# Performance work log

Hardware: AMD Instinct MI355X
Metric: run time of the kernel (lower is better)

The kernel has to match this reference:

```python
import jax, jax.numpy as jnp
import numpy as np

B, NPTS, T, P, C, D = 2, 32768, 32768, 512, 4, 768


def _sincos_pos_embed(centers, embed_dim):
    # centers: np [P,3]; matches get_3d_sincos_pos_embed
    c = centers - centers.mean(axis=0)
    c = c / np.linalg.norm(c, axis=1).max()
    div = np.exp(np.arange(0, embed_dim, 6) * -(np.log(10000.0) / embed_dim))  # [D/6]
    arg = c[:, None, :] * div[None, :, None]                                   # [P, D/6, 3]
    pe = np.concatenate([np.sin(arg), np.cos(arg)], axis=-1).reshape(centers.shape[0], embed_dim)
    return pe.astype(np.float32)


def setup_inputs() -> dict:
    key = jax.random.key(0)
    ks = jax.random.split(key, 12)
    rng = np.random.default_rng(0)

    # ragged patch sizes (avg 64) summing exactly to T
    sizes = rng.integers(32, 97, size=P).astype(np.int64)
    sizes = np.maximum((sizes * (T / sizes.sum())).astype(np.int64), 1)
    sizes[-1] += T - sizes.sum()
    patch_offset = jnp.asarray(np.concatenate([[0], np.cumsum(sizes)]), dtype=jnp.int32)  # [P+1]

    patch_index = jax.random.randint(ks[0], (T,), 0, NPTS, dtype=jnp.int32)
    latent = jax.random.normal(ks[1], (B, NPTS, C), dtype=jnp.float32)

    s = 0.02
    params = dict(
        w1a=jax.random.normal(ks[2], (C, D), jnp.float32) * s,
        b1a=jnp.zeros((D,), jnp.float32),
        w1b=jax.random.normal(ks[3], (D, D), jnp.float32) * s,
        b1b=jnp.zeros((D,), jnp.float32),
        w2a=jax.random.normal(ks[4], (2 * D, D), jnp.float32) * s,
        b2a=jnp.zeros((D,), jnp.float32),
        g2=jnp.ones((D,), jnp.float32),
        beta2=jnp.zeros((D,), jnp.float32),
        w2b=jax.random.normal(ks[5], (D, D), jnp.float32) * s,
        b2b=jnp.zeros((D,), jnp.float32),
    )

    centers = rng.standard_normal((P, 3))
    pos_embed = jnp.asarray(_sincos_pos_embed(centers, D))[None]  # [1, P, D]

    return dict(latent=latent, patch_index=patch_index, patch_offset=patch_offset,
                pos_embed=pos_embed, **params)


def _ln(x, eps, gamma=None, beta=None):
    mu = x.mean(axis=-1, keepdims=True)
    var = ((x - mu) ** 2).mean(axis=-1, keepdims=True)
    y = (x - mu) * jax.lax.rsqrt(var + eps)
    if gamma is not None:
        y = y * gamma + beta
    return y


def reference(latent, patch_index, patch_offset, pos_embed,
              w1a, b1a, w1b, b1b, w2a, b2a, g2, beta2, w2b, b2b):
    T_ = patch_index.shape[0]
    P_ = patch_offset.shape[0] - 1
    # segment id of each token (repeat_interleave inverse): seg[t] = patch containing t
    seg = jnp.searchsorted(patch_offset[1:], jnp.arange(T_, dtype=patch_offset.dtype), side='right')

    x = latent[:, patch_index, :]                           # [B, T, C] gather
    h = x @ w1a + b1a
    h = jax.nn.gelu(_ln(h, 1e-6), approximate=False)
    h = h @ w1b + b1b                                       # [B, T, D]

    segmax = lambda a: jax.ops.segment_max(a, seg, num_segments=P_)
    y = jax.vmap(segmax)(h)                                 # [B, P, D] ragged max-pool

    h2 = jnp.concatenate([y[:, seg, :], h], axis=-1)        # repeat_interleave + concat
    h2 = h2 @ w2a + b2a
    h2 = jax.nn.gelu(_ln(h2, 1e-5, g2, beta2), approximate=False)
    h2 = h2 @ w2b + b2b                                     # [B, T, D]
    raw_latent = h2

    out = jax.vmap(segmax)(raw_latent) + pos_embed          # [B, P, D]
    return out.astype(raw_latent.dtype), raw_latent
```

## Files before the change

kernel.cpp:

```cpp
#include <hip/hip_runtime.h>
#include <hip/hip_bf16.h>
#include <math.h>

#define B_    2
#define NPTS_ 32768
#define T_    32768
#define P_    512
#define C_    4
#define D_    768
#define M_    (B_ * T_)

typedef __bf16 bf16_t;
typedef __bf16 bf16x8 __attribute__((ext_vector_type(8)));
typedef __bf16 bf16x4 __attribute__((ext_vector_type(4)));
typedef float  f32x4  __attribute__((ext_vector_type(4)));

__device__ inline void gload16(const void* g, void* l) {
  __builtin_amdgcn_global_load_lds(
      (const __attribute__((address_space(1))) void*)g,
      (__attribute__((address_space(3))) void*)l, 16, 0, 0);
}

__device__ inline float gelu_exact(float x) {
  return 0.5f * x * (1.0f + erff(x * 0.70710678118654752f));
}

__device__ inline unsigned fmap(float x) {
  unsigned u = __float_as_uint(x);
  return (u & 0x80000000u) ? ~u : (u | 0x80000000u);
}
__device__ inline float funmap(unsigned u) {
  unsigned v = (u & 0x80000000u) ? (u & 0x7FFFFFFFu) : ~u;
  return __uint_as_float(v);
}

__global__ __launch_bounds__(256) void bigprep_kernel(
    const float4* __restrict__ latent4, const int* __restrict__ pidx,
    const float* __restrict__ w1a, const float* __restrict__ b1a,
    bf16_t* __restrict__ act1,
    const int* __restrict__ off, int* __restrict__ seg, uint4* __restrict__ umax,
    const float* __restrict__ w1b, const float* __restrict__ w2a,
    const float* __restrict__ w2b, const float* __restrict__ b1b,
    bf16_t* __restrict__ wBig, bf16_t* __restrict__ w2aTT,
    bf16_t* __restrict__ w2aBT, bf16_t* __restrict__ w2bT,
    bf16_t* __restrict__ w1bR, float* __restrict__ bBig) {
  int bid = blockIdx.x, tid = threadIdx.x;
  if (bid < 4096) {
    int wid = tid >> 6, lane = tid & 63;
    int mb = bid * 16 + wid * 4;
    int d8 = lane * 8, d4 = 512 + lane * 4;
    float bb[12], wreg[4][12];
    {
      float4 a0 = *(const float4*)(b1a + d8);
      float4 a1 = *(const float4*)(b1a + d8 + 4);
      float4 a2 = *(const float4*)(b1a + d4);
      bb[0]=a0.x; bb[1]=a0.y; bb[2]=a0.z; bb[3]=a0.w;
      bb[4]=a1.x; bb[5]=a1.y; bb[6]=a1.z; bb[7]=a1.w;
      bb[8]=a2.x; bb[9]=a2.y; bb[10]=a2.z; bb[11]=a2.w;
    }
    #pragma unroll
    for (int k = 0; k < 4; ++k) {
      const float* w = w1a + k * D_;
      float4 w0 = *(const float4*)(w + d8);
      float4 w1 = *(const float4*)(w + d8 + 4);
      float4 w2 = *(const float4*)(w + d4);
      wreg[k][0]=w0.x; wreg[k][1]=w0.y; wreg[k][2]=w0.z; wreg[k][3]=w0.w;
      wreg[k][4]=w1.x; wreg[k][5]=w1.y; wreg[k][6]=w1.z; wreg[k][7]=w1.w;
      wreg[k][8]=w2.x; wreg[k][9]=w2.y; wreg[k][10]=w2.z; wreg[k][11]=w2.w;
    }
    for (int rr = 0; rr < 4; ++rr) {
      int m = mb + rr;
      int b = m >> 15, t = m & (T_ - 1);
      float4 x = latent4[(size_t)b * NPTS_ + pidx[t]];
      float xk[4] = {x.x, x.y, x.z, x.w};
      float v[12];
      #pragma unroll
      for (int j = 0; j < 12; ++j) {
        v[j] = bb[j];
        #pragma unroll
        for (int k = 0; k < 4; ++k) v[j] += xk[k] * wreg[k][j];
      }
      float sum = 0.f, sq = 0.f;
      #pragma unroll
      for (int j = 0; j < 12; ++j) { sum += v[j]; sq += v[j]*v[j]; }
      #pragma unroll
      for (int o = 32; o > 0; o >>= 1) { sum += __shfl_xor(sum, o); sq += __shfl_xor(sq, o); }
      float mu = sum * (1.0f / D_);
      float rstd = rsqrtf(sq * (1.0f / D_) - mu * mu + 1e-6f);
      bf16x8 o8; bf16x4 o4;
      #pragma unroll
      for (int j = 0; j < 8; ++j) o8[j] = (bf16_t)gelu_exact((v[j] - mu) * rstd);
      #pragma unroll
      for (int j = 0; j < 4; ++j) o4[j] = (bf16_t)gelu_exact((v[8 + j] - mu) * rstd);
      size_t base = (size_t)m * D_;
      *(bf16x8*)(act1 + base + d8) = o8;
      *(bf16x4*)(act1 + base + d4) = o4;
    }
  } else if (bid < 6400) {
    __shared__ float tile[32][33];
    int r = bid - 4096;
    const float* src; bf16_t* dst;
    int which = r / 576; r -= which * 576;
    if (which == 0)      { src = w1b;             dst = wBig;  }
    else if (which == 1) { src = w2a;             dst = w2aTT; }
    else if (which == 2) { src = w2a + D_ * D_;   dst = w2aBT; }
    else                 { src = w2b;             dst = w2bT;  }
    int n0 = (r % 24) * 32, k0 = (r / 24) * 32;
    int tx = tid & 31, ty = tid >> 5;
    #pragma unroll
    for (int i = 0; i < 4; ++i)
      tile[ty + 8 * i][tx] = src[(size_t)(k0 + ty + 8 * i) * D_ + n0 + tx];
    __syncthreads();
    #pragma unroll
    for (int i = 0; i < 4; ++i)
      dst[(size_t)(n0 + ty + 8 * i) * D_ + k0 + tx] = (bf16_t)tile[tx][ty + 8 * i];
  } else if (bid < 6688) {
    size_t i8 = ((size_t)(bid - 6400) * 256 + tid) * 8;
    float4 a = *(const float4*)(w1b + i8);
    float4 b = *(const float4*)(w1b + i8 + 4);
    bf16x8 o;
    o[0]=(bf16_t)a.x; o[1]=(bf16_t)a.y; o[2]=(bf16_t)a.z; o[3]=(bf16_t)a.w;
    o[4]=(bf16_t)b.x; o[5]=(bf16_t)b.y; o[6]=(bf16_t)b.z; o[7]=(bf16_t)b.w;
    *(bf16x8*)(w1bR + i8) = o;
  } else if (bid < 6691) {
    int n = (bid - 6688) * 256 + tid;
    bBig[n] = b1b[n];
  } else if (bid < 6819) {
    int t = (bid - 6691) * 256 + tid;
    int lo = 0, hi = P_;
    while (lo < hi) {
      int mid = (lo + hi) >> 1;
      if (off[mid + 1] <= t) lo = mid + 1; else hi = mid;
    }
    seg[t] = lo;
  } else {
    umax[(size_t)(bid - 6819) * 256 + tid] = make_uint4(0, 0, 0, 0);
  }
}

__global__ __launch_bounds__(256) void bcombo_kernel(
    const float* __restrict__ b1b, const bf16_t* __restrict__ WcT,
    float* __restrict__ bc) {
  int n = blockIdx.x * 256 + threadIdx.x;
  float s = 0.f;
  for (int k = 0; k < D_; k += 8) {
    bf16x8 w = *(const bf16x8*)(WcT + (size_t)n * D_ + k);
    #pragma unroll
    for (int j = 0; j < 8; ++j) s += b1b[k + j] * (float)w[j];
  }
  bc[n] = s;
}

__global__ __launch_bounds__(256) void ln2_kernel(
    bf16_t* __restrict__ h2, const float* __restrict__ z,
    const int* __restrict__ seg, const float* __restrict__ g2,
    const float* __restrict__ beta2) {
  int wid = threadIdx.x >> 6, lane = threadIdx.x & 63;
  int m = blockIdx.x * 4 + wid;
  int b = m >> 15, t = m & (T_ - 1);
  int d8 = lane * 8, d4 = 512 + lane * 4;
  size_t base = (size_t)m * D_;
  const float* zrow = z + (size_t)((b << 9) + seg[t]) * D_;
  bf16x8 i8 = *(const bf16x8*)(h2 + base + d8);
  bf16x4 i4 = *(const bf16x4*)(h2 + base + d4);
  float4 z0 = *(const float4*)(zrow + d8);
  float4 z1 = *(const float4*)(zrow + d8 + 4);
  float4 z2 = *(const float4*)(zrow + d4);
  float v[12];
  #pragma unroll
  for (int j = 0; j < 8; ++j) v[j] = (float)i8[j];
  #pragma unroll
  for (int j = 0; j < 4; ++j) v[8 + j] = (float)i4[j];
  v[0]+=z0.x; v[1]+=z0.y; v[2]+=z0.z; v[3]+=z0.w;
  v[4]+=z1.x; v[5]+=z1.y; v[6]+=z1.z; v[7]+=z1.w;
  v[8]+=z2.x; v[9]+=z2.y; v[10]+=z2.z; v[11]+=z2.w;
  float sum = 0.f, sq = 0.f;
  #pragma unroll
  for (int j = 0; j < 12; ++j) { sum += v[j]; sq += v[j]*v[j]; }
  #pragma unroll
  for (int o = 32; o > 0; o >>= 1) { sum += __shfl_xor(sum, o); sq += __shfl_xor(sq, o); }
  float mu = sum * (1.0f / D_);
  float rstd = rsqrtf(sq * (1.0f / D_) - mu * mu + 1e-5f);
  float4 ga = *(const float4*)(g2 + d8);
  float4 gb = *(const float4*)(g2 + d8 + 4);
  float4 gc = *(const float4*)(g2 + d4);
  float4 ba = *(const float4*)(beta2 + d8);
  float4 bbv = *(const float4*)(beta2 + d8 + 4);
  float4 bc = *(const float4*)(beta2 + d4);
  float g[12] = {ga.x,ga.y,ga.z,ga.w, gb.x,gb.y,gb.z,gb.w, gc.x,gc.y,gc.z,gc.w};
  float be[12]= {ba.x,ba.y,ba.z,ba.w, bbv.x,bbv.y,bbv.z,bbv.w, bc.x,bc.y,bc.z,bc.w};
  bf16x8 o8; bf16x4 o4;
  #pragma unroll
  for (int j = 0; j < 8; ++j) o8[j] = (bf16_t)gelu_exact((v[j] - mu) * rstd * g[j] + be[j]);
  #pragma unroll
  for (int j = 0; j < 4; ++j) o4[j] = (bf16_t)gelu_exact((v[8+j] - mu) * rstd * g[8+j] + be[8+j]);
  *(bf16x8*)(h2 + base + d8) = o8;
  *(bf16x4*)(h2 + base + d4) = o4;
}

__global__ __launch_bounds__(256) void yconv_kernel(
    const uint4* __restrict__ ymax, bf16_t* __restrict__ y) {
  int t = blockIdx.x * 256 + threadIdx.x;
  uint4 u = ymax[t];
  bf16x4 o;
  o[0] = (bf16_t)funmap(u.x); o[1] = (bf16_t)funmap(u.y);
  o[2] = (bf16_t)funmap(u.z); o[3] = (bf16_t)funmap(u.w);
  *(bf16x4*)(y + (size_t)t * 4) = o;
}

__global__ __launch_bounds__(256) void final2_kernel(
    const uint4* __restrict__ rmax, const float4* __restrict__ pe,
    float4* __restrict__ out) {
  int t = blockIdx.x * 256 + threadIdx.x;
  int row = t / 192, col = t % 192;
  uint4 u = rmax[t];
  float4 p = pe[(row & (P_ - 1)) * 192 + col];
  float4 o;
  o.x = funmap(u.x) + p.x; o.y = funmap(u.y) + p.y;
  o.z = funmap(u.z) + p.z; o.w = funmap(u.w) + p.w;
  out[t] = o;
}

#define STAGE_A(P2, KTG)                                                     \
  { _Pragma("unroll")                                                        \
    for (int h = 0; h < 2; ++h) {                                            \
      _Pragma("unroll")                                                      \
      for (int ps = 0; ps < 2; ++ps) {                                       \
        int c = ps * 512 + wid * 64 + lane;                                  \
        int rw = c >> 3;                                                     \
        int cs = (c & 7) ^ (rw & 7);                                         \
        gload16(A + (size_t)(m0 + h * 128 + rw) * 768 + (KTG) + cs * 8,      \
                lds + (P2) * 65536 + h * 16384 + ps * 8192 + wid * 1024);    \
      } } }

#define STAGE_B(P2, KTG)                                                     \
  { _Pragma("unroll")                                                        \
    for (int h = 0; h < 2; ++h) {                                            \
      _Pragma("unroll")                                                      \
      for (int ps = 0; ps < 2; ++ps) {                                       \
        int c = ps * 512 + wid * 64 + lane;                                  \
        int rw = c >> 3;                                                     \
        int cs = (c & 7) ^ (rw & 7);                                         \
        gload16(BT + (size_t)(n0 + h * 128 + rw) * 768 + (KTG) + cs * 8,     \
                lds + (P2) * 65536 + 32768 + h * 16384 + ps * 8192 + wid * 1024); \
      } } }

#define READ_AF0(BASE)                                                       \
  { _Pragma("unroll")                                                        \
    for (int i = 0; i < 4; ++i) {                                            \
      _Pragma("unroll")                                                      \
      for (int s = 0; s < 2; ++s) {                                          \
        int row = i * 16 + lr;                                               \
        int ch = (s * 4 + hi) ^ cx;                                          \
        af0[i][s] = *(const bf16x8*)((BASE) + wm * 16384 + row * 128 + ch * 16); \
      } } }

#define READ_BF0(BASE)                                                       \
  { _Pragma("unroll")                                                        \
    for (int jb = 0; jb < 2; ++jb) {                                         \
      _Pragma("unroll")                                                      \
      for (int s = 0; s < 2; ++s) {                                          \
        int nrow = wn * 64 + jb * 16 + lr;                                   \
        int ch = (s * 4 + hi) ^ cx;                                          \
        bf0[jb][s] = *(const bf16x8*)((BASE) + 32768 + (nrow >> 7) * 16384 + \
                                      (nrow & 127) * 128 + ch * 16);         \
      } } }

template <int MODE, bool HASBIAS, typename OutT>
__global__ __launch_bounds__(512, 1) void gemm256_kernel(
    const bf16_t* __restrict__ A, const bf16_t* __restrict__ BT,
    const float* __restrict__ bias, OutT* __restrict__ C,
    const int* __restrict__ seg, unsigned* __restrict__ gmax) {
  constexpr int NT = 12;
  __shared__ __align__(16) char lds[131072];
  __shared__ int segm[256];
  int tid = threadIdx.x;
  int wid = tid >> 6, lane = tid & 63;
  int lr = lane & 15, hi = lane >> 4;
  int wm = wid >> 2, wn = wid & 3;

  int gx = gridDim.x;
  int nb = gx * gridDim.y;
  int bid = blockIdx.y * gx + blockIdx.x;
  int w = ((nb & 7) == 0) ? ((bid & 7) * (nb >> 3) + (bid >> 3)) : bid;
  int bx = w % gx, by = w / gx;
  int n0 = bx * 256, m0 = by * 256;

  if (MODE != 0) { if (tid < 256) segm[tid] = seg[(m0 + tid) & (T_ - 1)]; }

  f32x4 acc[8][4] = {};
  bf16x8 af0[4][2], af1[4][2], bf0[2][2], bf1[2][2];
  int cx = lr & 7;

  STAGE_A(0, 0); STAGE_B(0, 0);
  STAGE_A(1, 64); STAGE_B(1, 64);
  asm volatile("s_waitcnt vmcnt(8)" ::: "memory");
  __builtin_amdgcn_s_barrier();
  READ_AF0(lds); READ_BF0(lds);

  for (int j = 0; j < NT; ++j) {
    const char* base  = lds + (j & 1) * 65536;
    const char* baseN = lds + ((j & 1) ^ 1) * 65536;

    #pragma unroll
    for (int i = 0; i < 4; ++i)
      #pragma unroll
      for (int s = 0; s < 2; ++s) {
        int row = 64 + i * 16 + lr;
        int ch = (s * 4 + hi) ^ cx;
        af1[i][s] = *(const bf16x8*)(base + wm * 16384 + row * 128 + ch * 16);
      }
    __builtin_amdgcn_s_setprio(1);
    #pragma unroll
    for (int i = 0; i < 4; ++i)
      #pragma unroll
      for (int jb = 0; jb < 2; ++jb)
        #pragma unroll
        for (int s = 0; s < 2; ++s)
          acc[i][jb] = __builtin_amdgcn_mfma_f32_16x16x32_bf16(bf0[jb][s], af0[i][s], acc[i][jb], 0, 0, 0);
    __builtin_amdgcn_s_setprio(0);
    __builtin_amdgcn_s_barrier();

    #pragma unroll
    for (int jb = 0; jb < 2; ++jb)
      #pragma unroll
      for (int s = 0; s < 2; ++s) {
        int nrow = wn * 64 + 32 + jb * 16 + lr;
        int ch = (s * 4 + hi) ^ cx;
        bf1[jb][s] = *(const bf16x8*)(base + 32768 + (nrow >> 7) * 16384 +
                                      (nrow & 127) * 128 + ch * 16);
      }
    __builtin_amdgcn_s_setprio(1);
    #pragma unroll
    for (int i = 0; i < 4; ++i)
      #pragma unroll
      for (int jb = 0; jb < 2; ++jb)
        #pragma unroll
        for (int s = 0; s < 2; ++s)
          acc[4 + i][jb] = __builtin_amdgcn_mfma_f32_16x16x32_bf16(bf0[jb][s], af1[i][s], acc[4 + i][jb], 0, 0, 0);
    __builtin_amdgcn_s_setprio(0);
    __builtin_amdgcn_s_barrier();

    if (j + 2 < NT) STAGE_A(j & 1, (j + 2) * 64);
    __builtin_amdgcn_s_setprio(1);
    #pragma unroll
    for (int i = 0; i < 4; ++i)
      #pragma unroll
      for (int jb = 0; jb < 2; ++jb)
        #pragma unroll
        for (int s = 0; s < 2; ++s)
          acc[i][2 + jb] = __builtin_amdgcn_mfma_f32_16x16x32_bf16(bf1[jb][s], af0[i][s], acc[i][2 + jb], 0, 0, 0);
    __builtin_amdgcn_s_setprio(0);

    if (j + 1 < NT) {
      if (j + 2 < NT) asm volatile("s_waitcnt vmcnt(4)" ::: "memory");
      else            asm volatile("s_waitcnt vmcnt(0)" ::: "memory");
      __builtin_amdgcn_s_barrier();
      READ_AF0(baseN); READ_BF0(baseN);
      if (j + 2 < NT) STAGE_B(j & 1, (j + 2) * 64);
    }
    __builtin_amdgcn_s_setprio(1);
    #pragma unroll
    for (int i = 0; i < 4; ++i)
      #pragma unroll
      for (int jb = 0; jb < 2; ++jb)
        #pragma unroll
        for (int s = 0; s < 2; ++s)
          acc[4 + i][2 + jb] = __builtin_amdgcn_mfma_f32_16x16x32_bf16(bf1[jb][s], af1[i][s], acc[4 + i][2 + jb], 0, 0, 0);
    __builtin_amdgcn_s_setprio(0);
    __builtin_amdgcn_s_barrier();
  }

  f32x4 bvv[4];
  #pragma unroll
  for (int jb = 0; jb < 4; ++jb) {
    if (HASBIAS) {
      const float* bp = bias + n0 + wn * 64 + jb * 16 + hi * 4;
      bvv[jb][0] = bp[0]; bvv[jb][1] = bp[1]; bvv[jb][2] = bp[2]; bvv[jb][3] = bp[3];
    } else {
      bvv[jb][0] = bvv[jb][1] = bvv[jb][2] = bvv[jb][3] = 0.f;
    }
  }

  bool is_h = (MODE == 2) && (bx < 3);
  if (!is_h) {
    int nc0 = (MODE == 2) ? n0 - 768 : n0;
    #pragma unroll
    for (int i = 0; i < 8; ++i) {
      size_t ro = (size_t)(m0 + wm * 128 + i * 16 + lr) * 768 + (nc0 + wn * 64 + hi * 4);
      #pragma unroll
      for (int jb = 0; jb < 4; ++jb) {
        f32x4 v = acc[i][jb] + bvv[jb];
        if constexpr (sizeof(OutT) == 4) {
          *reinterpret_cast<f32x4*>(C + ro + jb * 16) = v;
        } else {
          bf16x4 o;
          #pragma unroll
          for (int r = 0; r < 4; ++r) o[r] = (bf16_t)v[r];
          *reinterpret_cast<bf16x4*>(C + ro + jb * 16) = o;
        }
      }
    }
  }

  if (MODE == 1 || is_h) {
    unsigned* smax = reinterpret_cast<unsigned*>(lds);
    __builtin_amdgcn_s_barrier();
    int sb = segm[0];
    int zb = (m0 >> 15) << 9;
    for (int q = tid; q < 16 * 256; q += 512) smax[q] = 0u;
    __syncthreads();

    int lrow = wm * 128 + lr;
    #pragma unroll
    for (int jb = 0; jb < 4; ++jb) {
      int nl = wn * 64 + jb * 16 + hi * 4;
      f32x4 run = acc[0][jb] + bvv[jb];
      int ps = segm[lrow];
      #pragma unroll
      for (int i = 1; i < 8; ++i) {
        int cs2 = segm[lrow + i * 16];
        f32x4 v = acc[i][jb] + bvv[jb];
        if (cs2 != ps) {
          #pragma unroll
          for (int r = 0; r < 4; ++r)
            atomicMax(&smax[(ps - sb) * 256 + nl + r], fmap(run[r]));
          run = v; ps = cs2;
        } else {
          #pragma unroll
          for (int r = 0; r < 4; ++r) run[r] = fmaxf(run[r], v[r]);
        }
      }
      #pragma unroll
      for (int r = 0; r < 4; ++r)
        atomicMax(&smax[(ps - sb) * 256 + nl + r], fmap(run[r]));
    }
    __syncthreads();

    int nseg = segm[255] - sb + 1;
    int mlo = m0 & (T_ - 1);
    bool strad_lo = (mlo != 0) && (seg[mlo - 1] == sb);
    bool strad_hi = (mlo + 256 < T_) && (seg[mlo + 256] == segm[255]);
    for (int q = tid; q < nseg * 256; q += 512) {
      int sl = q >> 8, nl2 = q & 255;
      unsigned val = smax[q];
      unsigned* dst = &gmax[(size_t)(zb + sb + sl) * 768 + n0 + nl2];
      bool bdry = (sl == 0 && strad_lo) || (sl == nseg - 1 && strad_hi);
      if (bdry) atomicMax(dst, val);
      else      *dst = val;
    }
  }
}

extern "C" void kernel_launch(void* const* d_in, const int* in_sizes, int n_in,
                              void* d_out, int out_size, void* d_ws, size_t ws_size,
                              hipStream_t stream) {
  const float* latent       = (const float*)d_in[0];
  const int*   patch_index  = (const int*)d_in[1];
  const int*   patch_offset = (const int*)d_in[2];
  const float* pos_embed    = (const float*)d_in[3];
  const float* w1a  = (const float*)d_in[4];
  const float* b1a  = (const float*)d_in[5];
  const float* w1b  = (const float*)d_in[6];
  const float* b1b  = (const float*)d_in[7];
  const float* w2a  = (const float*)d_in[8];
  const float* b2a  = (const float*)d_in[9];
  const float* g2   = (const float*)d_in[10];
  const float* beta2= (const float*)d_in[11];
  const float* w2b  = (const float*)d_in[12];
  const float* b2b  = (const float*)d_in[13];

  float* out_f   = (float*)d_out;
  float* raw_out = out_f + (size_t)B_ * P_ * D_;

  char* ws = (char*)d_ws;
  size_t off = 0;
  auto take = [&](size_t bytes) {
    off = (off + 255) & ~(size_t)255;
    char* p = ws + off;
    off += bytes;
    return p;
  };
  int*      seg   = (int*)     take((size_t)T_ * 4);
  bf16_t*   wBig  = (bf16_t*)  take((size_t)2 * D_ * D_ * 2);
  bf16_t*   w2aTT = (bf16_t*)  take((size_t)D_ * D_ * 2);
  bf16_t*   w2aBT = (bf16_t*)  take((size_t)D_ * D_ * 2);
  bf16_t*   w2bT  = (bf16_t*)  take((size_t)D_ * D_ * 2);
  bf16_t*   w1bR  = (bf16_t*)  take((size_t)D_ * D_ * 2);
  float*    bBig  = (float*)   take((size_t)2 * D_ * 4);
  bf16_t*   ybuf  = (bf16_t*)  take((size_t)B_ * P_ * D_ * 2);
  float*    zbuf  = (float*)   take((size_t)B_ * P_ * D_ * 4);
  unsigned* umax  = (unsigned*)take((size_t)2 * B_ * P_ * D_ * 4);
  unsigned* ymax  = umax;
  unsigned* rmax  = umax + (size_t)B_ * P_ * D_;
  bf16_t*   bufY  = (bf16_t*)  take((size_t)M_ * D_ * 2);
  size_t needX = (size_t)M_ * D_ * 2;
  size_t offX  = (off + 255) & ~(size_t)255;
  bf16_t* bufX;
  if (offX + needX <= ws_size) {
    bufX = (bf16_t*)take(needX);
  } else {
    bufX = (bf16_t*)raw_out;
  }

  bigprep_kernel<<<8355, 256, 0, stream>>>(
      (const float4*)latent, patch_index, w1a, b1a, bufX,
      patch_offset, seg, (uint4*)umax,
      w1b, w2a, w2b, b1b,
      wBig, w2aTT, w2aBT, w2bT, w1bR, bBig);

  gemm256_kernel<0, false, bf16_t><<<dim3(3, 3), 512, 0, stream>>>(
      w2aBT, w1bR, nullptr, wBig + (size_t)D_ * D_, nullptr, nullptr);

  bcombo_kernel<<<3, 256, 0, stream>>>(b1b, wBig + (size_t)D_ * D_, bBig + D_);

  gemm256_kernel<2, true, bf16_t><<<dim3(6, M_/256), 512, 0, stream>>>(
      bufX, wBig, bBig, bufY, seg, ymax);

  yconv_kernel<<<(B_ * P_ * D_) / (4 * 256), 256, 0, stream>>>(
      (const uint4*)ymax, ybuf);

  gemm256_kernel<0, true, float><<<dim3(3, (B_*P_)/256), 512, 0, stream>>>(
      ybuf, w2aTT, b2a, zbuf, nullptr, nullptr);

  ln2_kernel<<<M_ / 4, 256, 0, stream>>>(bufY, zbuf, seg, g2, beta2);

  gemm256_kernel<1, true, float><<<dim3(3, M_/256), 512, 0, stream>>>(
      bufY, w2bT, b2b, raw_out, seg, rmax);

  final2_kernel<<<768, 256, 0, stream>>>(
      (const uint4*)rmax, (const float4*)pos_embed, (float4*)out_f);
}
```

Before: 498.8 us.

## Fold weight-combo GEMM and bias into prep kernel; fuse y decode into fp32 z GEMM

Computes the combined weight product w1b·w2a_bottom and its bias term with scalar fp32 tiled loops inside the big prep kernel. This removes a separate small GEMM launch, the bcombo launch and the bf16 copy of w1b. It also replaces the yconv pass plus the bf16 MFMA GEMM for z with one fp32 SIMT tiled kernel that decodes the ordered-uint max values directly. The gain is fewer launches and intermediate buffers, at the cost of slower non-tensor-core arithmetic on these small GEMMs and extra serial work in the prep blocks.

```diff
diff --git a/kernel.cpp b/kernel.cpp
--- a/kernel.cpp
+++ b/kernel.cpp
@@ -43,7 +43,8 @@
     const float* __restrict__ w2b, const float* __restrict__ b1b,
     bf16_t* __restrict__ wBig, bf16_t* __restrict__ w2aTT,
     bf16_t* __restrict__ w2aBT, bf16_t* __restrict__ w2bT,
-    bf16_t* __restrict__ w1bR, float* __restrict__ bBig) {
+    float* __restrict__ bBig) {
+  __shared__ float tile2[2][32][33];
   int bid = blockIdx.x, tid = threadIdx.x;
   if (bid < 4096) {
     int wid = tid >> 6, lane = tid & 63;
@@ -97,7 +98,6 @@
       *(bf16x4*)(act1 + base + d4) = o4;
     }
   } else if (bid < 6400) {
-    __shared__ float tile[32][33];
     int r = bid - 4096;
     const float* src; bf16_t* dst;
     int which = r / 576; r -= which * 576;
@@ -109,24 +109,46 @@
     int tx = tid & 31, ty = tid >> 5;
     #pragma unroll
     for (int i = 0; i < 4; ++i)
-      tile[ty + 8 * i][tx] = src[(size_t)(k0 + ty + 8 * i) * D_ + n0 + tx];
+      tile2[0][ty + 8 * i][tx] = src[(size_t)(k0 + ty + 8 * i) * D_ + n0 + tx];
     __syncthreads();
     #pragma unroll
     for (int i = 0; i < 4; ++i)
-      dst[(size_t)(n0 + ty + 8 * i) * D_ + k0 + tx] = (bf16_t)tile[tx][ty + 8 * i];
-  } else if (bid < 6688) {
-    size_t i8 = ((size_t)(bid - 6400) * 256 + tid) * 8;
-    float4 a = *(const float4*)(w1b + i8);
-    float4 b = *(const float4*)(w1b + i8 + 4);
-    bf16x8 o;
-    o[0]=(bf16_t)a.x; o[1]=(bf16_t)a.y; o[2]=(bf16_t)a.z; o[3]=(bf16_t)a.w;
-    o[4]=(bf16_t)b.x; o[5]=(bf16_t)b.y; o[6]=(bf16_t)b.z; o[7]=(bf16_t)b.w;
-    *(bf16x8*)(w1bR + i8) = o;
-  } else if (bid < 6691) {
-    int n = (bid - 6688) * 256 + tid;
+      dst[(size_t)(n0 + ty + 8 * i) * D_ + k0 + tx] = (bf16_t)tile2[0][tx][ty + 8 * i];
+  } else if (bid < 6976) {
+    int r = bid - 6400;
+    int n0 = (r / 24) * 32, k0 = (r % 24) * 32;
+    int tx = tid & 31, ty = tid >> 5;
+    float acc[4] = {0.f, 0.f, 0.f, 0.f};
+    for (int j0 = 0; j0 < D_; j0 += 32) {
+      __syncthreads();
+      #pragma unroll
+      for (int i = 0; i < 4; ++i) {
+        tile2[0][ty + 8 * i][tx] = w1b[(size_t)(k0 + ty + 8 * i) * D_ + j0 + tx];
+        tile2[1][ty + 8 * i][tx] = w2a[(size_t)(D_ + j0 + ty + 8 * i) * D_ + n0 + tx];
+      }
+      __syncthreads();
+      #pragma unroll
+      for (int jj = 0; jj < 32; ++jj) {
+        float av = tile2[0][tx][jj];
+        #pragma unroll
+        for (int i = 0; i < 4; ++i)
+          acc[i] += av * tile2[1][jj][ty + 8 * i];
+      }
+    }
+    bf16_t* WcT = wBig + (size_t)D_ * D_;
+    #pragma unroll
+    for (int i = 0; i < 4; ++i)
+      WcT[(size_t)(n0 + ty + 8 * i) * D_ + k0 + tx] = (bf16_t)acc[i];
+  } else if (bid < 6979) {
+    int n = (bid - 6976) * 256 + tid;
     bBig[n] = b1b[n];
-  } else if (bid < 6819) {
-    int t = (bid - 6691) * 256 + tid;
+  } else if (bid < 6982) {
+    int n = (bid - 6979) * 256 + tid;
+    float s = 0.f;
+    for (int k = 0; k < D_; ++k) s += b1b[k] * w2a[(size_t)(D_ + k) * D_ + n];
+    bBig[D_ + n] = s;
+  } else if (bid < 7110) {
+    int t = (bid - 6982) * 256 + tid;
     int lo = 0, hi = P_;
     while (lo < hi) {
       int mid = (lo + hi) >> 1;
@@ -134,21 +156,37 @@
     }
     seg[t] = lo;
   } else {
-    umax[(size_t)(bid - 6819) * 256 + tid] = make_uint4(0, 0, 0, 0);
-  }
-}
-
-__global__ __launch_bounds__(256) void bcombo_kernel(
-    const float* __restrict__ b1b, const bf16_t* __restrict__ WcT,
-    float* __restrict__ bc) {
-  int n = blockIdx.x * 256 + threadIdx.x;
-  float s = 0.f;
-  for (int k = 0; k < D_; k += 8) {
-    bf16x8 w = *(const bf16x8*)(WcT + (size_t)n * D_ + k);
-    #pragma unroll
-    for (int j = 0; j < 8; ++j) s += b1b[k + j] * (float)w[j];
-  }
-  bc[n] = s;
+    umax[(size_t)(bid - 7110) * 256 + tid] = make_uint4(0, 0, 0, 0);
+  }
+}
+
+__global__ __launch_bounds__(256) void zvec_kernel(
+    const unsigned* __restrict__ ymax, const float* __restrict__ w2a,
+    const float* __restrict__ b2a, float* __restrict__ z) {
+  __shared__ float Aw[32][33], Bw[32][33];
+  int r = blockIdx.x;
+  int m0 = (r / 24) * 32, n0 = (r % 24) * 32;
+  int tx = threadIdx.x & 31, ty = threadIdx.x >> 5;
+  float acc[4] = {0.f, 0.f, 0.f, 0.f};
+  for (int k0 = 0; k0 < D_; k0 += 32) {
+    __syncthreads();
+    #pragma unroll
+    for (int i = 0; i < 4; ++i) {
+      Aw[ty + 8 * i][tx] = funmap(ymax[(size_t)(m0 + ty + 8 * i) * D_ + k0 + tx]);
+      Bw[ty + 8 * i][tx] = w2a[(size_t)(k0 + ty + 8 * i) * D_ + n0 + tx];
+    }
+    __syncthreads();
+    #pragma unroll
+    for (int kk = 0; kk < 32; ++kk) {
+      float bv = Bw[kk][tx];
+      #pragma unroll
+      for (int i = 0; i < 4; ++i) acc[i] += Aw[ty + 8 * i][kk] * bv;
+    }
+  }
+  float bav = b2a[n0 + tx];
+  #pragma unroll
+  for (int i = 0; i < 4; ++i)
+    z[(size_t)(m0 + ty + 8 * i) * D_ + n0 + tx] = acc[i] + bav;
 }
 
 __global__ __launch_bounds__(256) void ln2_kernel(
@@ -196,16 +234,6 @@
   for (int j = 0; j < 4; ++j) o4[j] = (bf16_t)gelu_exact((v[8+j] - mu) * rstd * g[8+j] + be[8+j]);
   *(bf16x8*)(h2 + base + d8) = o8;
   *(bf16x4*)(h2 + base + d4) = o4;
-}
-
-__global__ __launch_bounds__(256) void yconv_kernel(
-    const uint4* __restrict__ ymax, bf16_t* __restrict__ y) {
-  int t = blockIdx.x * 256 + threadIdx.x;
-  uint4 u = ymax[t];
-  bf16x4 o;
-  o[0] = (bf16_t)funmap(u.x); o[1] = (bf16_t)funmap(u.y);
-  o[2] = (bf16_t)funmap(u.z); o[3] = (bf16_t)funmap(u.w);
-  *(bf16x4*)(y + (size_t)t * 4) = o;
 }
 
 __global__ __launch_bounds__(256) void final2_kernel(
@@ -486,9 +514,7 @@
   bf16_t*   w2aTT = (bf16_t*)  take((size_t)D_ * D_ * 2);
   bf16_t*   w2aBT = (bf16_t*)  take((size_t)D_ * D_ * 2);
   bf16_t*   w2bT  = (bf16_t*)  take((size_t)D_ * D_ * 2);
-  bf16_t*   w1bR  = (bf16_t*)  take((size_t)D_ * D_ * 2);
   float*    bBig  = (float*)   take((size_t)2 * D_ * 4);
-  bf16_t*   ybuf  = (bf16_t*)  take((size_t)B_ * P_ * D_ * 2);
   float*    zbuf  = (float*)   take((size_t)B_ * P_ * D_ * 4);
   unsigned* umax  = (unsigned*)take((size_t)2 * B_ * P_ * D_ * 4);
   unsigned* ymax  = umax;
@@ -503,25 +529,16 @@
     bufX = (bf16_t*)raw_out;
   }
 
-  bigprep_kernel<<<8355, 256, 0, stream>>>(
+  bigprep_kernel<<<8646, 256, 0, stream>>>(
       (const float4*)latent, patch_index, w1a, b1a, bufX,
       patch_offset, seg, (uint4*)umax,
       w1b, w2a, w2b, b1b,
-      wBig, w2aTT, w2aBT, w2bT, w1bR, bBig);
-
-  gemm256_kernel<0, false, bf16_t><<<dim3(3, 3), 512, 0, stream>>>(
-      w2aBT, w1bR, nullptr, wBig + (size_t)D_ * D_, nullptr, nullptr);
-
-  bcombo_kernel<<<3, 256, 0, stream>>>(b1b, wBig + (size_t)D_ * D_, bBig + D_);
+      wBig, w2aTT, w2aBT, w2bT, bBig);
 
   gemm256_kernel<2, true, bf16_t><<<dim3(6, M_/256), 512, 0, stream>>>(
       bufX, wBig, bBig, bufY, seg, ymax);
 
-  yconv_kernel<<<(B_ * P_ * D_) / (4 * 256), 256, 0, stream>>>(
-      (const uint4*)ymax, ybuf);
-
-  gemm256_kernel<0, true, float><<<dim3(3, (B_*P_)/256), 512, 0, stream>>>(
-      ybuf, w2aTT, b2a, zbuf, nullptr, nullptr);
+  zvec_kernel<<<768, 256, 0, stream>>>(ymax, w2a, b2a, zbuf);
 
   ln2_kernel<<<M_ / 4, 256, 0, stream>>>(bufY, zbuf, seg, g2, beta2);
 
```

New measurement: 526.3 us. +5.5%, slower.
